# Kernel tuning notes

Measured on AMD Instinct MI355X. Metric: run time of the kernel, lower is better.

The kernel has to match this reference:

```python
import jax, jax.numpy as jnp
import numpy as np

N = 50000
D = 256
K = 16  # fixed neighbor-list degree (regularized form of the ragged edge_dict)


def setup_inputs() -> dict:
    key = jax.random.key(0)
    k1, k2, k3, k4 = jax.random.split(key, 4)
    feats = jax.random.normal(k1, (N, D), dtype=jnp.float32)
    edge_dict = jax.random.randint(k2, (N, K), 0, N)  # int32 neighbor indices
    W = jax.random.normal(k3, (D, D), dtype=jnp.float32) * (1.0 / np.sqrt(D))
    b = jax.random.normal(k4, (D,), dtype=jnp.float32) * 0.01
    idx = jnp.arange(N)
    sadj = jnp.zeros((1,), dtype=jnp.float32)
    epoch = 0
    return {"idx": idx, "feats": feats, "edge_dict": edge_dict,
            "sadj": sadj, "epoch": epoch, "W": W, "b": b}


def reference(idx, feats, edge_dict, sadj, epoch, W, b):
    # fc -> relu (dropout is identity in eval mode; p=0.5 train-only)
    x = jax.nn.relu(feats @ W.T + b)  # [N, D]
    # region_aggregate: per-node mean over fixed-degree neighbor lists
    pooled = jnp.mean(x[edge_dict], axis=1)  # gather [N, K, D] -> mean -> [N, D]
    return pooled
```

## Files before the change

### kernel.cpp

```cpp
#include <hip/hip_runtime.h>
#include <hip/hip_bf16.h>

#define NN  50000
#define DD  256
#define KNB 16
#define BM  64
#define NSL 8
#define SLW 32
#define NKT 8

typedef __attribute__((ext_vector_type(8))) short bf16x8;
typedef __attribute__((ext_vector_type(4))) float f32x4;

static __device__ __forceinline__ float bf2f(unsigned int u16) {
    union { unsigned int i; float f; } c; c.i = u16 << 16; return c.f;
}
static __device__ __forceinline__ float bf2f_hi(unsigned int u) {
    union { unsigned int i; float f; } c; c.i = u & 0xffff0000u; return c.f;
}
static __device__ __forceinline__ short f2bf(float f) {
    union { float f; unsigned int i; } c; c.f = f;
    unsigned int r = c.i + 0x7FFFu + ((c.i >> 16) & 1u);
    return (short)(r >> 16);
}
static __device__ __forceinline__ bf16x8 pack8(float4 a, float4 b) {
    union { __hip_bfloat162 h[4]; bf16x8 v; } u;
    u.h[0] = __float22bfloat162_rn(make_float2(a.x, a.y));
    u.h[1] = __float22bfloat162_rn(make_float2(a.z, a.w));
    u.h[2] = __float22bfloat162_rn(make_float2(b.x, b.y));
    u.h[3] = __float22bfloat162_rn(make_float2(b.z, b.w));
    return u.v;
}

#define GLOAD_LDS16(g, l) \
    __builtin_amdgcn_global_load_lds((const __attribute__((address_space(1))) unsigned int*)(g), \
                                     (__attribute__((address_space(3))) unsigned int*)(l), 16, 0, 0)

__global__ void convert_w(const float* __restrict__ W, unsigned short* __restrict__ Wbf)
{
    int s = blockIdx.x * blockDim.x + threadIdx.x;
    if (s >= 8192) return;
    int j  = s & 15;
    int kb = (s >> 4) & 3;
    int nb = (s >> 6) & 15;
    int kt = s >> 10;
    const float4* p = (const float4*)(W + (nb * 16 + j) * DD + kt * 32 + kb * 8);
    *(bf16x8*)&Wbf[(size_t)s * 8] = pack8(p[0], p[1]);
}

__global__ __launch_bounds__(256, 4) void gemm_relu(
    const float* __restrict__ feats, const unsigned short* __restrict__ Wbf,
    const float* __restrict__ bias, unsigned short* __restrict__ xs)
{
    __shared__ short At[2][BM * 32];
    __shared__ short Wt[2][8192];

    const int tid  = threadIdx.x;
    const int lane = tid & 63;
    const int wc   = tid >> 6;
    const int l15  = lane & 15;
    const int lg   = lane >> 4;
    const int blockRow = blockIdx.x * BM;

    const int arow = tid >> 2, akq = tid & 3;
    const int grow = blockRow + arow;
    const bool aval = grow < NN;
    const float* abase = feats + (size_t)grow * DD + akq * 8;
    const int aslot = (((arow >> 4) * 4 + akq) * 16 + (arow & 15)) * 8;

    float4 ra, rb;
    auto aload = [&](int kt) {
        if (aval) {
            const float4* p = (const float4*)(abase + kt * 32);
            ra = p[0]; rb = p[1];
        } else { ra = make_float4(0,0,0,0); rb = ra; }
    };
    auto astore = [&](int buf) {
        *(bf16x8*)&At[buf][aslot] = pack8(ra, rb);
    };
    auto wstage = [&](int kt, int buf) {
        const char* src = (const char*)Wbf + kt * 16384 + tid * 16;
        char* dst = (char*)&Wt[buf][0] + tid * 16;
        #pragma unroll
        for (int c = 0; c < 4; ++c)
            GLOAD_LDS16(src + c * 4096, dst + c * 4096);
    };

    float bv[4];
    #pragma unroll
    for (int n = 0; n < 4; ++n) bv[n] = bias[wc * 64 + n * 16 + l15];

    f32x4 acc[4][4];
    #pragma unroll
    for (int m = 0; m < 4; ++m)
        #pragma unroll
        for (int n = 0; n < 4; ++n) acc[m][n] = (f32x4)0.0f;

    aload(0); wstage(0, 0); astore(0);
    __syncthreads();

    int cur = 0;
    for (int kt = 0; kt < NKT; ++kt) {
        int nxt = cur ^ 1;
        if (kt + 1 < NKT) { aload(kt + 1); wstage(kt + 1, nxt); }

        bf16x8 afr[4], bfr[4];
        #pragma unroll
        for (int m = 0; m < 4; ++m)
            afr[m] = *(const bf16x8*)&At[cur][((m * 4 + lg) * 16 + l15) * 8];
        #pragma unroll
        for (int n = 0; n < 4; ++n)
            bfr[n] = *(const bf16x8*)&Wt[cur][(((wc * 4 + n) * 4 + lg) * 16 + l15) * 8];

        #pragma unroll
        for (int m = 0; m < 4; ++m)
            #pragma unroll
            for (int n = 0; n < 4; ++n)
                acc[m][n] = __builtin_amdgcn_mfma_f32_16x16x32_bf16(
                    afr[m], bfr[n], acc[m][n], 0, 0, 0);

        if (kt + 1 < NKT) astore(nxt);
        __syncthreads();
        cur = nxt;
    }

    #pragma unroll
    for (int n = 0; n < 4; ++n) {
        const int sl = wc * 2 + (n >> 1);
        const int c  = (n & 1) * 16 + l15;
        unsigned short* xb = xs + (size_t)sl * NN * SLW + c;
        #pragma unroll
        for (int m = 0; m < 4; ++m) {
            int rbase = blockRow + m * 16 + (lg << 2);
            f32x4 a = acc[m][n];
            #pragma unroll
            for (int r = 0; r < 4; ++r) {
                int row = rbase + r;
                if (row < NN) {
                    float vv = fmaxf(a[r] + bv[n], 0.0f);
                    xb[(size_t)row * SLW] = (unsigned short)f2bf(vv);
                }
            }
        }
    }
}

__global__ __launch_bounds__(256) void gather_mean(
    const int* __restrict__ edge, const unsigned short* __restrict__ xs,
    float* __restrict__ out)
{
    const int s    = blockIdx.x & 7;
    const int grp  = blockIdx.x >> 3;
    const int lane = threadIdx.x & 63;
    const int w    = threadIdx.x >> 6;
    const int iw0  = grp * 64 + w * 16;
    const int g    = lane >> 2, q = lane & 3;
    const int i    = iw0 + g;

    int eoff = iw0 * KNB + lane * 4;
    if (eoff > NN * KNB - 4) eoff = NN * KNB - 4;
    int4 e4 = *(const int4*)(edge + eoff);
    int e[4] = { e4.x, e4.y, e4.z, e4.w };

    const unsigned short* xsl = xs + (size_t)s * NN * SLW;

    float a[8];
    #pragma unroll
    for (int j = 0; j < 8; ++j) a[j] = 0.0f;

    #pragma unroll
    for (int k = 0; k < KNB; ++k) {
        int src = (lane & 60) | (k >> 2);
        int n = __shfl(e[k & 3], src, 64);
        bf16x8 v = *(const bf16x8*)(xsl + (size_t)n * SLW + q * 8);
        const unsigned int* vu = (const unsigned int*)&v;
        #pragma unroll
        for (int j = 0; j < 4; ++j) {
            a[2 * j]     += bf2f(vu[j] & 0xffffu);
            a[2 * j + 1] += bf2f_hi(vu[j]);
        }
    }

    if (i < NN) {
        f32x4 o0 = { a[0] * 0.0625f, a[1] * 0.0625f, a[2] * 0.0625f, a[3] * 0.0625f };
        f32x4 o1 = { a[4] * 0.0625f, a[5] * 0.0625f, a[6] * 0.0625f, a[7] * 0.0625f };
        float* op = out + (size_t)i * DD + s * SLW + q * 8;
        __builtin_nontemporal_store(o0, (f32x4*)op);
        __builtin_nontemporal_store(o1, (f32x4*)(op + 4));
    }
}

extern "C" void kernel_launch(void* const* d_in, const int* in_sizes, int n_in,
                              void* d_out, int out_size, void* d_ws, size_t ws_size,
                              hipStream_t stream) {
    const float* feats = (const float*)d_in[1];
    const int*   edge  = (const int*)d_in[2];
    const float* W     = (const float*)d_in[5];
    const float* b     = (const float*)d_in[6];
    float* out = (float*)d_out;

    unsigned short* xs  = (unsigned short*)d_ws;
    unsigned short* Wbf = (unsigned short*)((char*)d_ws + (size_t)NN * DD * 2);

    const int ngrp = (NN + 63) / 64;
    convert_w<<<dim3(32), dim3(256), 0, stream>>>(W, Wbf);
    gemm_relu<<<dim3(ngrp), dim3(256), 0, stream>>>(feats, Wbf, b, xs);
    gather_mean<<<dim3(ngrp * NSL), dim3(256), 0, stream>>>(edge, xs, out);
}
```

Measured before the change: 65.22 us.

## Preload full A tile into LDS upfront; gather loads edge list directly

The GEMM kernel now loads and converts the whole 64x256 feature tile to bf16 in LDS once before the k-loop. It no longer double-buffers A per k-step with register staging, and the k-loop is fully unrolled. Launch bounds drop to 2 blocks per SM, since LDS use roughly doubles. The gather kernel drops the cross-lane shuffle and has each lane load its node's 16 neighbor indices itself with nontemporal loads, trading redundant index loads (four lanes per node) for fewer shuffles.

```diff
diff --git a/kernel.cpp b/kernel.cpp
--- a/kernel.cpp
+++ b/kernel.cpp
@@ -11,6 +11,7 @@
 
 typedef __attribute__((ext_vector_type(8))) short bf16x8;
 typedef __attribute__((ext_vector_type(4))) float f32x4;
+typedef __attribute__((ext_vector_type(4))) int   i32x4;
 
 static __device__ __forceinline__ float bf2f(unsigned int u16) {
     union { unsigned int i; float f; } c; c.i = u16 << 16; return c.f;
@@ -48,11 +49,11 @@
     *(bf16x8*)&Wbf[(size_t)s * 8] = pack8(p[0], p[1]);
 }
 
-__global__ __launch_bounds__(256, 4) void gemm_relu(
+__global__ __launch_bounds__(256, 2) void gemm_relu(
     const float* __restrict__ feats, const unsigned short* __restrict__ Wbf,
     const float* __restrict__ bias, unsigned short* __restrict__ xs)
 {
-    __shared__ short At[2][BM * 32];
+    __shared__ short At[16384];
     __shared__ short Wt[2][8192];
 
     const int tid  = threadIdx.x;
@@ -62,22 +63,6 @@
     const int lg   = lane >> 4;
     const int blockRow = blockIdx.x * BM;
 
-    const int arow = tid >> 2, akq = tid & 3;
-    const int grow = blockRow + arow;
-    const bool aval = grow < NN;
-    const float* abase = feats + (size_t)grow * DD + akq * 8;
-    const int aslot = (((arow >> 4) * 4 + akq) * 16 + (arow & 15)) * 8;
-
-    float4 ra, rb;
-    auto aload = [&](int kt) {
-        if (aval) {
-            const float4* p = (const float4*)(abase + kt * 32);
-            ra = p[0]; rb = p[1];
-        } else { ra = make_float4(0,0,0,0); rb = ra; }
-    };
-    auto astore = [&](int buf) {
-        *(bf16x8*)&At[buf][aslot] = pack8(ra, rb);
-    };
     auto wstage = [&](int kt, int buf) {
         const char* src = (const char*)Wbf + kt * 16384 + tid * 16;
         char* dst = (char*)&Wt[buf][0] + tid * 16;
@@ -86,6 +71,31 @@
             GLOAD_LDS16(src + c * 4096, dst + c * 4096);
     };
 
+    wstage(0, 0);
+    {
+        const int r = tid >> 2, q = tid & 3;
+        int row = blockRow + r; if (row > NN - 1) row = NN - 1;
+        const float* base = feats + (size_t)row * DD;
+        const int m = r >> 4, i15 = r & 15;
+        #pragma unroll
+        for (int h = 0; h < 4; ++h) {
+            float4 v[4];
+            #pragma unroll
+            for (int j = 0; j < 4; ++j)
+                v[j] = *(const float4*)(base + h * 64 + j * 16 + q * 4);
+            #pragma unroll
+            for (int j = 0; j < 4; ++j) {
+                int k0 = h * 64 + j * 16 + q * 4;
+                int kt = k0 >> 5, kq = (k0 >> 3) & 3, eo = k0 & 7;
+                union { __hip_bfloat162 h2[2]; uint2 u; } p;
+                p.h2[0] = __float22bfloat162_rn(make_float2(v[j].x, v[j].y));
+                p.h2[1] = __float22bfloat162_rn(make_float2(v[j].z, v[j].w));
+                int el = (((kt * 4 + m) * 4 + kq) * 16 + i15) * 8 + eo;
+                *(uint2*)&At[el] = p.u;
+            }
+        }
+    }
+
     float bv[4];
     #pragma unroll
     for (int n = 0; n < 4; ++n) bv[n] = bias[wc * 64 + n * 16 + l15];
@@ -96,18 +106,17 @@
         #pragma unroll
         for (int n = 0; n < 4; ++n) acc[m][n] = (f32x4)0.0f;
 
-    aload(0); wstage(0, 0); astore(0);
     __syncthreads();
 
-    int cur = 0;
+    #pragma unroll
     for (int kt = 0; kt < NKT; ++kt) {
-        int nxt = cur ^ 1;
-        if (kt + 1 < NKT) { aload(kt + 1); wstage(kt + 1, nxt); }
+        const int cur = kt & 1;
+        if (kt + 1 < NKT) wstage(kt + 1, cur ^ 1);
 
         bf16x8 afr[4], bfr[4];
         #pragma unroll
         for (int m = 0; m < 4; ++m)
-            afr[m] = *(const bf16x8*)&At[cur][((m * 4 + lg) * 16 + l15) * 8];
+            afr[m] = *(const bf16x8*)&At[(((kt * 4 + m) * 4 + lg) * 16 + l15) * 8];
         #pragma unroll
         for (int n = 0; n < 4; ++n)
             bfr[n] = *(const bf16x8*)&Wt[cur][(((wc * 4 + n) * 4 + lg) * 16 + l15) * 8];
@@ -119,9 +128,7 @@
                 acc[m][n] = __builtin_amdgcn_mfma_f32_16x16x32_bf16(
                     afr[m], bfr[n], acc[m][n], 0, 0, 0);
 
-        if (kt + 1 < NKT) astore(nxt);
         __syncthreads();
-        cur = nxt;
     }
 
     #pragma unroll
@@ -153,16 +160,20 @@
     const int grp  = blockIdx.x >> 3;
     const int lane = threadIdx.x & 63;
     const int w    = threadIdx.x >> 6;
-    const int iw0  = grp * 64 + w * 16;
     const int g    = lane >> 2, q = lane & 3;
-    const int i    = iw0 + g;
-
-    int eoff = iw0 * KNB + lane * 4;
-    if (eoff > NN * KNB - 4) eoff = NN * KNB - 4;
-    int4 e4 = *(const int4*)(edge + eoff);
-    int e[4] = { e4.x, e4.y, e4.z, e4.w };
+    const int i    = grp * 64 + w * 16 + g;
+    int il = i; if (il > NN - 1) il = NN - 1;
+
+    const i32x4* ep = (const i32x4*)(edge + (size_t)il * KNB);
+    i32x4 e0 = __builtin_nontemporal_load(ep);
+    i32x4 e1 = __builtin_nontemporal_load(ep + 1);
+    i32x4 e2 = __builtin_nontemporal_load(ep + 2);
+    i32x4 e3 = __builtin_nontemporal_load(ep + 3);
+    int e[16] = { e0[0], e0[1], e0[2], e0[3], e1[0], e1[1], e1[2], e1[3],
+                  e2[0], e2[1], e2[2], e2[3], e3[0], e3[1], e3[2], e3[3] };
 
     const unsigned short* xsl = xs + (size_t)s * NN * SLW;
+    const unsigned qo = q * 8;
 
     float a[8];
     #pragma unroll
@@ -170,9 +181,8 @@
 
     #pragma unroll
     for (int k = 0; k < KNB; ++k) {
-        int src = (lane & 60) | (k >> 2);
-        int n = __shfl(e[k & 3], src, 64);
-        bf16x8 v = *(const bf16x8*)(xsl + (size_t)n * SLW + q * 8);
+        unsigned off = (unsigned)e[k] * SLW + qo;
+        bf16x8 v = *(const bf16x8*)(xsl + off);
         const unsigned int* vu = (const unsigned int*)&v;
         #pragma unroll
         for (int j = 0; j < 4; ++j) {
```

Measured after the change: 83.82 us. +28.5%, slower.
